# Performance work log

Hardware: AMD Instinct MI355X
Metric: run time of the kernel (lower is better)

## Reference

```python
import jax, jax.numpy as jnp
import numpy as np

EMB, HID, E, TOPK = 1024, 4096, 8, 2

def setup_inputs() -> dict:
    key = jax.random.key(0)
    ks = jax.random.split(key, 10)
    s = 0.02
    return {
        "x":   jax.random.normal(ks[0], (4, 2048, EMB), jnp.float32),
        # router MLP: Linear(EMB,HID) -> SiLU -> Linear(HID,E)
        "rw1": s * jax.random.normal(ks[1], (EMB, HID), jnp.float32),
        "rb1": jnp.zeros((HID,), jnp.float32),
        "rw2": s * jax.random.normal(ks[2], (HID, E), jnp.float32),
        "rb2": jnp.zeros((E,), jnp.float32),
        # stacked expert MLPs: Linear(EMB,HID) -> SiLU -> Linear(HID,EMB)
        "w1":  s * jax.random.normal(ks[3], (E, EMB, HID), jnp.float32),
        "b1":  jnp.zeros((E, HID), jnp.float32),
        "w2":  s * jax.random.normal(ks[4], (E, HID, EMB), jnp.float32),
        "b2":  jnp.zeros((E, EMB), jnp.float32),
    }

def reference(x, rw1, rb1, rw2, rb2, w1, b1, w2, b2):
    B, S, D = x.shape
    # Router: logits over experts, top-k, softmax over the k selected logits
    logits = jax.nn.silu(jnp.einsum('bsd,dh->bsh', x, rw1) + rb1)
    logits = jnp.einsum('bsh,he->bse', logits, rw2) + rb2
    k_logits, k_index = jax.lax.top_k(logits, TOPK)          # [B,S,K]
    k_prob = jax.nn.softmax(k_logits, axis=-1)               # [B,S,K]

    xf = x.reshape(B * S, D)                                 # [T,D]
    k_index_f = k_index.reshape(B * S, TOPK)
    k_prob_f = k_prob.reshape(B * S, TOPK)

    out = jnp.zeros_like(xf)
    for e in range(E):  # small fixed expert count
        # per-token combine weight for expert e (0 if not routed)
        we = jnp.sum(jnp.where(k_index_f == e, k_prob_f, 0.0), axis=-1)  # [T]
        h = jax.nn.silu(xf @ w1[e] + b1[e]) @ w2[e] + b2[e]              # [T,D]
        out = out + we[:, None] * h
    return out.reshape(B, S, D)
```

## Files before the change

kernel.cpp:

```cpp
#include <hip/hip_runtime.h>
#include <stdint.h>

#define TOK 8192
#define EMBD 1024
#define HIDD 4096
#define NEXP 8

typedef _Float16 f16;
typedef _Float16 f16x8 __attribute__((ext_vector_type(8)));
typedef _Float16 f16x4 __attribute__((ext_vector_type(4)));
typedef float f32x4 __attribute__((ext_vector_type(4)));
typedef unsigned short u16;
typedef unsigned short u16x4 __attribute__((ext_vector_type(4)));

constexpr size_t OFF_X16   = 0;
constexpr size_t OFF_RW1T  = OFF_X16  + (size_t)TOK*EMBD*2;
constexpr size_t OFF_W1T   = OFF_RW1T + (size_t)HIDD*EMBD*2;
constexpr size_t OFF_W2T   = OFF_W1T  + (size_t)NEXP*HIDD*EMBD*2;
constexpr size_t OFF_HR    = OFF_W2T  + (size_t)NEXP*EMBD*HIDD*2;
constexpr size_t OFF_HG    = OFF_HR   + (size_t)TOK*HIDD*2;
constexpr size_t OFF_YG    = OFF_HG   + (size_t)(2*TOK+256)*HIDD*2;
constexpr size_t OFF_XF    = OFF_YG   + (size_t)(2*TOK+256)*EMBD*2;
constexpr size_t OFF_HF    = OFF_XF   + 512UL*EMBD*4;
constexpr size_t OFF_KIDX  = OFF_HF   + 512UL*HIDD*4;
constexpr size_t OFF_KW    = OFF_KIDX + 2UL*TOK*4;
constexpr size_t OFF_RMAP  = OFF_KW   + 2UL*TOK*4;
constexpr size_t OFF_TMAP  = OFF_RMAP + 2UL*TOK*4;
constexpr size_t OFF_FLAG  = OFF_TMAP + 2UL*TOK*4;
constexpr size_t OFF_MISC  = OFF_FLAG + 512UL*4;
constexpr size_t OFF_RW2T  = OFF_MISC + 1024;
constexpr size_t WS_TOTAL  = OFF_RW2T + (size_t)NEXP*HIDD*2;

__device__ __align__(1024) unsigned char g_ws[WS_TOTAL];

__device__ __forceinline__ u16 f2h(float f) {
  f16 h = (f16)f;
  return __builtin_bit_cast(u16, h);
}

__device__ __forceinline__ void async_cp16(const void* g, void* l) {
  __builtin_amdgcn_global_load_lds((const __attribute__((address_space(1))) void*)g,
                                   (__attribute__((address_space(3))) void*)l, 16, 0, 0);
}

__global__ void k_prep(const float* __restrict__ x, const float* __restrict__ rw2) {
  int b = blockIdx.x, tid = threadIdx.x;
  constexpr int NBX = TOK * EMBD / 1024;
  if (b < NBX) {
    u16* X16 = (u16*)(g_ws + OFF_X16);
    int i = (b * 256 + tid) * 4;
    float4 v = *(const float4*)(x + i);
    u16x4 o;
    o[0] = f2h(v.x); o[1] = f2h(v.y); o[2] = f2h(v.z); o[3] = f2h(v.w);
    *(u16x4*)(X16 + i) = o;
  } else if (b < NBX + HIDD / 256) {
    u16* RW2T = (u16*)(g_ws + OFF_RW2T);
    int h = (b - NBX) * 256 + tid;
    float4 a = *(const float4*)&rw2[(size_t)h * 8];
    float4 bb = *(const float4*)&rw2[(size_t)h * 8 + 4];
    RW2T[0 * HIDD + h] = f2h(a.x);
    RW2T[1 * HIDD + h] = f2h(a.y);
    RW2T[2 * HIDD + h] = f2h(a.z);
    RW2T[3 * HIDD + h] = f2h(a.w);
    RW2T[4 * HIDD + h] = f2h(bb.x);
    RW2T[5 * HIDD + h] = f2h(bb.y);
    RW2T[6 * HIDD + h] = f2h(bb.z);
    RW2T[7 * HIDD + h] = f2h(bb.w);
  } else {
    if (tid < 32) ((int*)(g_ws + OFF_MISC))[tid] = 0;
  }
}

template <int R, int C>
__device__ __forceinline__ void tpose(const float* __restrict__ src, u16* __restrict__ dst,
                                      int bx, int by, u16 (*t)[68]) {
  int r0 = by * 64, c0 = bx * 64;
  int tid = threadIdx.x;
#pragma unroll
  for (int i = 0; i < 4; ++i) {
    int r = i * 16 + (tid >> 4);
    int c4 = (tid & 15) * 4;
    float4 v = *(const float4*)&src[(size_t)(r0 + r) * C + c0 + c4];
    u16x4 p;
    p[0] = f2h(v.x); p[1] = f2h(v.y); p[2] = f2h(v.z); p[3] = f2h(v.w);
    *(u16x4*)&t[r][c4 ^ (((r >> 2) & 15) << 2)] = p;
  }
  __syncthreads();
#pragma unroll
  for (int i = 0; i < 4; ++i) {
    int lin = i * 256 + tid;
    int cc = lin >> 4;
    int q = lin & 15;
    int rr0 = q * 4;
    int cs = cc ^ (q << 2);
    u16x4 o;
    o[0] = t[rr0 + 0][cs];
    o[1] = t[rr0 + 1][cs];
    o[2] = t[rr0 + 2][cs];
    o[3] = t[rr0 + 3][cs];
    *(u16x4*)&dst[(size_t)(c0 + cc) * R + r0 + rr0] = o;
  }
}

__global__ void k_transpose_all(const float* __restrict__ rw1, const float* __restrict__ w1,
                                const float* __restrict__ w2) {
  __shared__ u16 t[64][68];
  int flat = blockIdx.x;
  if (flat < 9 * 1024) {
    int m = flat >> 10, rem = flat & 1023;
    int bx = rem & 63, by = rem >> 6;
    const float* src = (m == 0) ? rw1 : w1 + (size_t)(m - 1) * EMBD * HIDD;
    u16* dst = (u16*)(g_ws + OFF_RW1T) + (size_t)m * HIDD * EMBD;
    tpose<EMBD, HIDD>(src, dst, bx, by, t);
  } else {
    int f2 = flat - 9 * 1024;
    int m = f2 >> 10, rem = f2 & 1023;
    int bx = rem & 15, by = rem >> 4;
    const float* src = w2 + (size_t)m * HIDD * EMBD;
    u16* dst = (u16*)(g_ws + OFF_W2T) + (size_t)m * EMBD * HIDD;
    tpose<HIDD, EMBD>(src, dst, bx, by, t);
  }
}

template <bool SILU, bool GROUPED, bool INDIRECT, int GN>
__global__ __launch_bounds__(512, 2) void gemm256(size_t offA, size_t offB,
                                                  const float* __restrict__ bias,
                                                  size_t offC, int Mfix, int N, int K) {
  const u16* A  = (const u16*)(g_ws + offA);
  const u16* BT = (const u16*)(g_ws + offB);
  u16* C = (u16*)(g_ws + offC);
  const int* offs = (const int*)(g_ws + OFF_MISC) + 8;
  const int* tokmap = (const int*)(g_ws + OFF_TMAP);

  int nx = gridDim.x, ny = gridDim.y;
  int nwg = nx * ny * gridDim.z;
  int flat = (blockIdx.z * ny + blockIdx.y) * nx + blockIdx.x;
  int cpx = nwg >> 3;
  int u = (flat & 7) * cpx + (flat >> 3);
  int bxin = u % GN;
  int t1 = u / GN;
  int by = t1 % ny;
  int t2 = t1 / ny;
  int nxg = nx / GN;
  int g = t2 % nxg;
  int bz = t2 / nxg;
  int bx = g * GN + bxin;

  int e = GROUPED ? bz : 0;
  int rbase = GROUPED ? offs[e] : 0;
  int Me = GROUPED ? (offs[e + 1] - rbase) : Mfix;
  int m0 = by * 256;
  if (m0 >= Me) return;
  int n0 = bx * 256;
  const u16* Be = BT + (size_t)e * N * K;
  const float* be = bias + (size_t)e * N;

  __shared__ __align__(128) u16 SM[65536];

  int tid = threadIdx.x;
  int lane = tid & 63, wid = tid >> 6;
  int wm = wid >> 2, wn = wid & 3;
  int rsel = lane & 15;
  int rg = lane >> 4;
  int sp0 = (rg ^ (rsel & 7)) * 8;

  int srow = tid >> 3;
  int cnom = tid & 7;
  int csrc = (cnom ^ (srow & 7)) * 8;

  const u16* aP[4];
  const u16* bP[4];
#pragma unroll
  for (int i = 0; i < 4; ++i) {
    int r = m0 + i * 64 + srow;
    if (GROUPED) r = (r < Me) ? r : (Me - 1);
    if (INDIRECT) aP[i] = A + (size_t)tokmap[rbase + r] * K + csrc;
    else          aP[i] = A + (size_t)(rbase + r) * K + csrc;
    bP[i] = Be + (size_t)(n0 + i * 64 + srow) * K + csrc;
  }

#define STAGE(b, k0)                                                        \
  do {                                                                      \
    _Pragma("unroll") for (int i = 0; i < 4; ++i)                           \
      async_cp16(aP[i] + (k0), &SM[(b)*16384 + (i * 512 + tid) * 8]);       \
    _Pragma("unroll") for (int i = 0; i < 4; ++i)                           \
      async_cp16(bP[i] + (k0), &SM[32768 + (b)*16384 + (i * 512 + tid) * 8]); \
  } while (0)

#define COMPUTE(bb)                                                             \
  {                                                                             \
    const u16* Ab = &SM[(bb)*16384];                                            \
    const u16* Bb = &SM[32768 + (bb)*16384];                                    \
    _Pragma("unroll") for (int ks = 0; ks < 2; ++ks) {                          \
      int spo = sp0 ^ (ks << 5);                                                \
      f16x8 af[8], bf[4];                                                       \
      _Pragma("unroll") for (int i = 0; i < 8; ++i)                             \
        af[i] = *(const f16x8*)&Ab[wm * 8192 + i * 1024 + rsel * 64 + spo];     \
      _Pragma("unroll") for (int j = 0; j < 4; ++j)                             \
        bf[j] = *(const f16x8*)&Bb[wn * 4096 + j * 1024 + rsel * 64 + spo];     \
      _Pragma("unroll") for (int i = 0; i < 8; ++i)                             \
        _Pragma("unroll") for (int j = 0; j < 4; ++j)                           \
          acc[i][j] = __builtin_amdgcn_mfma_f32_16x16x32_f16(af[i], bf[j],      \
                                                             acc[i][j], 0, 0, 0); \
    }                                                                           \
  }

  f32x4 acc[8][4] = {};
  int nt = K >> 6;

  STAGE(0, 0);
  asm volatile("s_waitcnt vmcnt(0)" ::: "memory");
  __builtin_amdgcn_s_barrier();

  int buf = 0;
  for (int t = 0; t < nt; ++t) {
    if (t + 1 < nt) STAGE(buf ^ 1, (t + 1) << 6);
    COMPUTE(buf);
    asm volatile("s_waitcnt vmcnt(0)" ::: "memory");
    __builtin_amdgcn_s_barrier();
    buf ^= 1;
  }
#undef COMPUTE
#undef STAGE

  u16* Cs = SM;
#pragma unroll
  for (int j = 0; j < 4; ++j) {
    int colL = wn * 64 + j * 16 + rsel;
    float bn = be[n0 + colL];
#pragma unroll
    for (int i = 0; i < 8; ++i) {
#pragma unroll
      for (int r = 0; r < 4; ++r) {
        int ml = wm * 128 + i * 16 + rg * 4 + r;
        float v = acc[i][j][r] + bn;
        if (SILU) v = v / (1.0f + __expf(-v));
        Cs[ml * 256 + colL] = f2h(v);
      }
    }
  }
  __syncthreads();
#pragma unroll
  for (int i = 0; i < 16; ++i) {
    int lin = i * 512 + tid;
    int row = lin >> 5, sl = lin & 31;
    if (!GROUPED || (m0 + row < Me))
      *(uint4*)(C + (size_t)(rbase + m0 + row) * N + n0 + sl * 8) =
          *(const uint4*)&Cs[row * 256 + sl * 8];
  }
}

__global__ void k_router(const float* __restrict__ rb2, const float* __restrict__ x) {
  const u16* HR = (const u16*)(g_ws + OFF_HR);
  const u16* RW2T = (const u16*)(g_ws + OFF_RW2T);
  int* kidx = (int*)(g_ws + OFF_KIDX);
  float* kw = (float*)(g_ws + OFF_KW);
  int* flag = (int*)(g_ws + OFF_FLAG);
  float* XF = (float*)(g_ws + OFF_XF);
  int* misc = (int*)(g_ws + OFF_MISC);

  int t = blockIdx.x, tid = threadIdx.x;
  int lane = tid & 63, w = tid >> 6;
  float acc[8] = {};
  const u16* hrow = HR + (size_t)t * HIDD;
#pragma unroll
  for (int i = 0; i < 2; ++i) {
    int base = i * 2048 + tid * 8;
    f16x8 v = *(const f16x8*)&hrow[base];
    float hv[8];
#pragma unroll
    for (int jj = 0; jj < 8; ++jj) hv[jj] = (float)v[jj];
#pragma unroll
    for (int e2 = 0; e2 < 8; ++e2) {
      f16x8 wv = *(const f16x8*)&RW2T[e2 * HIDD + base];
#pragma unroll
      for (int jj = 0; jj < 8; ++jj) acc[e2] += hv[jj] * (float)wv[jj];
    }
  }
#pragma unroll
  for (int m = 1; m < 64; m <<= 1)
#pragma unroll
    for (int e2 = 0; e2 < 8; ++e2) acc[e2] += __shfl_xor(acc[e2], m);

  __shared__ float red[4][8];
  __shared__ int s_fi;
  if (lane == 0)
    for (int e2 = 0; e2 < 8; ++e2) red[w][e2] = acc[e2];
  if (tid == 0) s_fi = -1;
  __syncthreads();
  if (tid == 0) {
    float lg[8];
    for (int e2 = 0; e2 < 8; ++e2)
      lg[e2] = red[0][e2] + red[1][e2] + red[2][e2] + red[3][e2] + rb2[e2];
    int i1 = 0; float l1 = lg[0];
    for (int e2 = 1; e2 < 8; ++e2) if (lg[e2] > l1) { l1 = lg[e2]; i1 = e2; }
    int i2 = -1; float l2 = -3.4e38f;
    for (int e2 = 0; e2 < 8; ++e2) if (e2 != i1 && lg[e2] > l2) { l2 = lg[e2]; i2 = e2; }
    float l3 = -3.4e38f;
    for (int e2 = 0; e2 < 8; ++e2) if (e2 != i1 && e2 != i2 && lg[e2] > l3) l3 = lg[e2];
    float ex = __expf(l2 - l1);
    float inv = 1.0f / (1.0f + ex);
    kidx[2 * t] = i1; kidx[2 * t + 1] = i2;
    kw[2 * t] = inv;  kw[2 * t + 1] = ex * inv;
    if (l2 - l3 < 4e-3f) {
      int fi = atomicAdd(misc + 30, 1);
      if (fi < 512) { flag[fi] = t; s_fi = fi; }
    }
  }
  __syncthreads();
  int fi = s_fi;
  if (fi >= 0) {
    const float* xs = x + (size_t)t * EMBD;
    float* xd = XF + (size_t)fi * EMBD;
    int d = tid * 4;
    *(float4*)(xd + d) = *(const float4*)(xs + d);
  }
}

__global__ __launch_bounds__(256) void k_flag_gemm(const float* __restrict__ rw1,
                                                   const float* __restrict__ rb1) {
  int* misc = (int*)(g_ws + OFF_MISC);
  int F = misc[30]; if (F > 512) F = 512;
  int m0 = blockIdx.y * 64;
  if (m0 >= F) return;
  int n0 = blockIdx.x * 64;
  const float* XF = (const float*)(g_ws + OFF_XF);
  float* HF = (float*)(g_ws + OFF_HF);
  __shared__ float As[64][17];
  __shared__ float Bs[16][65];
  int tid = threadIdx.x;
  float acc[4][4] = {};
  for (int k0 = 0; k0 < EMBD; k0 += 16) {
#pragma unroll
    for (int i = 0; i < 4; ++i) {
      int lin = i * 256 + tid;
      As[lin >> 4][lin & 15] = XF[(size_t)(m0 + (lin >> 4)) * EMBD + k0 + (lin & 15)];
      Bs[lin >> 6][lin & 63] = rw1[(size_t)(k0 + (lin >> 6)) * HIDD + n0 + (lin & 63)];
    }
    __syncthreads();
    int ty = tid >> 4, tx = tid & 15;
#pragma unroll
    for (int kk = 0; kk < 16; ++kk) {
      float a4[4], b4[4];
#pragma unroll
      for (int a = 0; a < 4; ++a) a4[a] = As[ty * 4 + a][kk];
#pragma unroll
      for (int b = 0; b < 4; ++b) b4[b] = Bs[kk][tx * 4 + b];
#pragma unroll
      for (int a = 0; a < 4; ++a)
#pragma unroll
        for (int b = 0; b < 4; ++b) acc[a][b] += a4[a] * b4[b];
    }
    __syncthreads();
  }
  int ty = tid >> 4, tx = tid & 15;
  for (int a = 0; a < 4; ++a)
    for (int b = 0; b < 4; ++b) {
      int n = n0 + tx * 4 + b;
      float v = acc[a][b] + rb1[n];
      v = v / (1.0f + __expf(-v));
      HF[(size_t)(m0 + ty * 4 + a) * HIDD + n] = v;
    }
}

__global__ void k_flag_fix(const float* __restrict__ rw2, const float* __restrict__ rb2) {
  int* misc = (int*)(g_ws + OFF_MISC);
  int F = misc[30]; if (F > 512) F = 512;
  int fi = blockIdx.x; if (fi >= F) return;
  const int* flag = (const int*)(g_ws + OFF_FLAG);
  const float* HF = (const float*)(g_ws + OFF_HF);
  int* kidx = (int*)(g_ws + OFF_KIDX);
  float* kw = (float*)(g_ws + OFF_KW);
  int t = flag[fi];
  int tid = threadIdx.x, lane = tid & 63, w = tid >> 6;
  const float* h = HF + (size_t)fi * HIDD;
  float acc[8] = {};
  for (int i = 0; i < 16; ++i) {
    int hh = i * 256 + tid;
    float hv = h[hh];
    const float* r2 = rw2 + (size_t)hh * 8;
#pragma unroll
    for (int e2 = 0; e2 < 8; ++e2) acc[e2] += hv * r2[e2];
  }
#pragma unroll
  for (int m = 1; m < 64; m <<= 1)
#pragma unroll
    for (int e2 = 0; e2 < 8; ++e2) acc[e2] += __shfl_xor(acc[e2], m);
  __shared__ float red[4][8];
  if (lane == 0)
    for (int e2 = 0; e2 < 8; ++e2) red[w][e2] = acc[e2];
  __syncthreads();
  if (tid == 0) {
    float lg[8];
    for (int e2 = 0; e2 < 8; ++e2)
      lg[e2] = red[0][e2] + red[1][e2] + red[2][e2] + red[3][e2] + rb2[e2];
    int i1 = 0; float l1 = lg[0];
    for (int e2 = 1; e2 < 8; ++e2) if (lg[e2] > l1) { l1 = lg[e2]; i1 = e2; }
    int i2 = -1; float l2 = -3.4e38f;
    for (int e2 = 0; e2 < 8; ++e2) if (e2 != i1 && lg[e2] > l2) { l2 = lg[e2]; i2 = e2; }
    float ex = __expf(l2 - l1);
    float inv = 1.0f / (1.0f + ex);
    kidx[2 * t] = i1; kidx[2 * t + 1] = i2;
    kw[2 * t] = inv;  kw[2 * t + 1] = ex * inv;
  }
}

__global__ __launch_bounds__(1024) void k_count_scan() {
  const int* kidx = (const int*)(g_ws + OFF_KIDX);
  int* misc = (int*)(g_ws + OFF_MISC);
  int tid = threadIdx.x;
  int c[8] = {};
  for (int i = tid; i < 2 * TOK; i += 1024) {
    int e = kidx[i];
#pragma unroll
    for (int k = 0; k < 8; ++k) c[k] += (e == k) ? 1 : 0;
  }
#pragma unroll
  for (int m = 1; m < 64; m <<= 1)
#pragma unroll
    for (int k = 0; k < 8; ++k) c[k] += __shfl_xor(c[k], m);
  __shared__ int red[16][8];
  int lane = tid & 63, w = tid >> 6;
  if (lane == 0)
#pragma unroll
    for (int k = 0; k < 8; ++k) red[w][k] = c[k];
  __syncthreads();
  if (tid == 0) {
    int* offs = misc + 8;
    int* cur = misc + 20;
    offs[0] = 0;
    for (int e = 0; e < 8; ++e) {
      int s = 0;
      for (int ww = 0; ww < 16; ++ww) s += red[ww][e];
      offs[e + 1] = offs[e] + s;
      cur[e] = offs[e];
    }
  }
}

__global__ void k_build() {
  int s = blockIdx.x * 256 + threadIdx.x;
  if (s < 2 * TOK) {
    const int* kidx = (const int*)(g_ws + OFF_KIDX);
    int* rowmap = (int*)(g_ws + OFF_RMAP);
    int* tokmap = (int*)(g_ws + OFF_TMAP);
    int* misc = (int*)(g_ws + OFF_MISC);
    int e = kidx[s];
    int r = atomicAdd(&misc[20 + e], 1);
    rowmap[s] = r;
    tokmap[r] = s >> 1;
  }
}

__global__ void k_combine(float* __restrict__ out) {
  int t = blockIdx.x, tid = threadIdx.x;
  const int* rowmap = (const int*)(g_ws + OFF_RMAP);
  const float* kw = (const float*)(g_ws + OFF_KW);
  const u16* YG = (const u16*)(g_ws + OFF_YG);
  int r0 = rowmap[2 * t], r1 = rowmap[2 * t + 1];
  float w0 = kw[2 * t], w1 = kw[2 * t + 1];
  int d = tid * 4;
  f16x4 a = *(const f16x4*)(YG + (size_t)r0 * EMBD + d);
  f16x4 b = *(const f16x4*)(YG + (size_t)r1 * EMBD + d);
  float4 o;
  o.x = w0 * (float)a[0] + w1 * (float)b[0];
  o.y = w0 * (float)a[1] + w1 * (float)b[1];
  o.z = w0 * (float)a[2] + w1 * (float)b[2];
  o.w = w0 * (float)a[3] + w1 * (float)b[3];
  *(float4*)(out + (size_t)t * EMBD + d) = o;
}

extern "C" void kernel_launch(void* const* d_in, const int* in_sizes, int n_in,
                              void* d_out, int out_size, void* d_ws, size_t ws_size,
                              hipStream_t stream) {
  const float* x   = (const float*)d_in[0];
  const float* rw1 = (const float*)d_in[1];
  const float* rb1 = (const float*)d_in[2];
  const float* rw2 = (const float*)d_in[3];
  const float* rb2 = (const float*)d_in[4];
  const float* w1  = (const float*)d_in[5];
  const float* b1  = (const float*)d_in[6];
  const float* w2  = (const float*)d_in[7];
  const float* b2  = (const float*)d_in[8];
  float* out = (float*)d_out;

  k_prep<<<dim3(TOK * EMBD / 1024 + HIDD / 256 + 1), dim3(256), 0, stream>>>(x, rw2);
  k_transpose_all<<<dim3(9 * 1024 + 8 * 1024), dim3(256), 0, stream>>>(rw1, w1, w2);
  gemm256<true, false, false, 4><<<dim3(HIDD / 256, TOK / 256, 1), dim3(512), 0, stream>>>(
      OFF_X16, OFF_RW1T, rb1, OFF_HR, TOK, HIDD, EMBD);
  k_router<<<dim3(TOK), dim3(256), 0, stream>>>(rb2, x);
  k_flag_gemm<<<dim3(HIDD / 64, 8), dim3(256), 0, stream>>>(rw1, rb1);
  k_flag_fix<<<dim3(512), dim3(256), 0, stream>>>(rw2, rb2);
  k_count_scan<<<dim3(1), dim3(1024), 0, stream>>>();
  k_build<<<dim3(2 * TOK / 256), dim3(256), 0, stream>>>();
  gemm256<true, true, true, 4><<<dim3(HIDD / 256, 2 * TOK / 256, 8), dim3(512), 0, stream>>>(
      OFF_X16, OFF_W1T, b1, OFF_HG, 0, HIDD, EMBD);
  gemm256<false, true, false, 1><<<dim3(EMBD / 256, 2 * TOK / 256, 8), dim3(512), 0, stream>>>(
      OFF_HG, OFF_W2T, b2, OFF_YG, 0, EMBD, HIDD);
  k_combine<<<dim3(TOK), dim3(256), 0, stream>>>(out);
}
```

Measured before the change: 810.7 us.

## Fuse router second linear into first router GEMM epilogue with partial logits

The router's HID->E projection now runs in the epilogue of the first router GEMM on the f16 tile already in LDS. Each block writes per-column-block partial logits instead of writing the full hidden activation to global memory. k_router becomes a light per-token kernel that sums 16 partials and does top-2. The flagged-token GEMM also reads x through the flag index instead of a copied buffer. This removes a large global write and reread of the router hidden activations, at the cost of a serial dot-product epilogue in the GEMM.

```diff
diff --git a/kernel.cpp b/kernel.cpp
--- a/kernel.cpp
+++ b/kernel.cpp
@@ -29,7 +29,8 @@
 constexpr size_t OFF_FLAG  = OFF_TMAP + 2UL*TOK*4;
 constexpr size_t OFF_MISC  = OFF_FLAG + 512UL*4;
 constexpr size_t OFF_RW2T  = OFF_MISC + 1024;
-constexpr size_t WS_TOTAL  = OFF_RW2T + (size_t)NEXP*HIDD*2;
+constexpr size_t OFF_LG    = OFF_RW2T + (size_t)NEXP*HIDD*2;
+constexpr size_t WS_TOTAL  = OFF_LG + 16UL*TOK*8*4;
 
 __device__ __align__(1024) unsigned char g_ws[WS_TOTAL];
 
@@ -122,7 +123,7 @@
   }
 }
 
-template <bool SILU, bool GROUPED, bool INDIRECT, int GN>
+template <bool SILU, bool GROUPED, bool INDIRECT, int GN, bool ROUTER>
 __global__ __launch_bounds__(512, 2) void gemm256(size_t offA, size_t offB,
                                                   const float* __restrict__ bias,
                                                   size_t offC, int Mfix, int N, int K) {
@@ -240,91 +241,97 @@
     }
   }
   __syncthreads();
-#pragma unroll
-  for (int i = 0; i < 16; ++i) {
-    int lin = i * 512 + tid;
-    int row = lin >> 5, sl = lin & 31;
-    if (!GROUPED || (m0 + row < Me))
-      *(uint4*)(C + (size_t)(rbase + m0 + row) * N + n0 + sl * 8) =
-          *(const uint4*)&Cs[row * 256 + sl * 8];
-  }
-}
-
-__global__ void k_router(const float* __restrict__ rb2, const float* __restrict__ x) {
-  const u16* HR = (const u16*)(g_ws + OFF_HR);
-  const u16* RW2T = (const u16*)(g_ws + OFF_RW2T);
+
+  if constexpr (ROUTER) {
+    float* LG = (float*)(g_ws + OFF_LG);
+    const u16* RW2T = (const u16*)(g_ws + OFF_RW2T);
+    int row = tid >> 1, half = tid & 1;
+    int cbase = half * 128;
+    int rot = (lane >> 1) & 15;
+    float a8[8];
+#pragma unroll
+    for (int ee = 0; ee < 8; ++ee) a8[ee] = 0.f;
+#pragma unroll
+    for (int ee = 0; ee < 8; ++ee) {
+      const u16* wrow = &RW2T[ee * HIDD + n0 + cbase];
+      float a = 0.f;
+      for (int i = 0; i < 16; ++i) {
+        int c8 = (i + rot) & 15;
+        f16x8 wv = *(const f16x8*)&wrow[c8 * 8];
+        f16x8 cv = *(const f16x8*)&Cs[row * 256 + cbase + c8 * 8];
+#pragma unroll
+        for (int j = 0; j < 8; ++j) a += (float)cv[j] * (float)wv[j];
+      }
+      a8[ee] = a;
+    }
+#pragma unroll
+    for (int ee = 0; ee < 8; ++ee) a8[ee] += __shfl_xor(a8[ee], 1);
+    if (half == 0) {
+      float* dst = LG + ((size_t)bx * TOK + (m0 + row)) * 8;
+      f32x4 lo, hi;
+      lo[0] = a8[0]; lo[1] = a8[1]; lo[2] = a8[2]; lo[3] = a8[3];
+      hi[0] = a8[4]; hi[1] = a8[5]; hi[2] = a8[6]; hi[3] = a8[7];
+      *(f32x4*)dst = lo;
+      *(f32x4*)(dst + 4) = hi;
+    }
+  } else {
+#pragma unroll
+    for (int i = 0; i < 16; ++i) {
+      int lin = i * 512 + tid;
+      int row = lin >> 5, sl = lin & 31;
+      if (!GROUPED || (m0 + row < Me))
+        *(uint4*)(C + (size_t)(rbase + m0 + row) * N + n0 + sl * 8) =
+            *(const uint4*)&Cs[row * 256 + sl * 8];
+    }
+  }
+}
+
+__global__ void k_router(const float* __restrict__ rb2) {
+  const float* LG = (const float*)(g_ws + OFF_LG);
   int* kidx = (int*)(g_ws + OFF_KIDX);
   float* kw = (float*)(g_ws + OFF_KW);
   int* flag = (int*)(g_ws + OFF_FLAG);
-  float* XF = (float*)(g_ws + OFF_XF);
   int* misc = (int*)(g_ws + OFF_MISC);
 
-  int t = blockIdx.x, tid = threadIdx.x;
-  int lane = tid & 63, w = tid >> 6;
-  float acc[8] = {};
-  const u16* hrow = HR + (size_t)t * HIDD;
-#pragma unroll
-  for (int i = 0; i < 2; ++i) {
-    int base = i * 2048 + tid * 8;
-    f16x8 v = *(const f16x8*)&hrow[base];
-    float hv[8];
-#pragma unroll
-    for (int jj = 0; jj < 8; ++jj) hv[jj] = (float)v[jj];
-#pragma unroll
-    for (int e2 = 0; e2 < 8; ++e2) {
-      f16x8 wv = *(const f16x8*)&RW2T[e2 * HIDD + base];
-#pragma unroll
-      for (int jj = 0; jj < 8; ++jj) acc[e2] += hv[jj] * (float)wv[jj];
-    }
-  }
-#pragma unroll
-  for (int m = 1; m < 64; m <<= 1)
-#pragma unroll
-    for (int e2 = 0; e2 < 8; ++e2) acc[e2] += __shfl_xor(acc[e2], m);
-
-  __shared__ float red[4][8];
-  __shared__ int s_fi;
-  if (lane == 0)
-    for (int e2 = 0; e2 < 8; ++e2) red[w][e2] = acc[e2];
-  if (tid == 0) s_fi = -1;
-  __syncthreads();
-  if (tid == 0) {
-    float lg[8];
-    for (int e2 = 0; e2 < 8; ++e2)
-      lg[e2] = red[0][e2] + red[1][e2] + red[2][e2] + red[3][e2] + rb2[e2];
-    int i1 = 0; float l1 = lg[0];
-    for (int e2 = 1; e2 < 8; ++e2) if (lg[e2] > l1) { l1 = lg[e2]; i1 = e2; }
-    int i2 = -1; float l2 = -3.4e38f;
-    for (int e2 = 0; e2 < 8; ++e2) if (e2 != i1 && lg[e2] > l2) { l2 = lg[e2]; i2 = e2; }
-    float l3 = -3.4e38f;
-    for (int e2 = 0; e2 < 8; ++e2) if (e2 != i1 && e2 != i2 && lg[e2] > l3) l3 = lg[e2];
-    float ex = __expf(l2 - l1);
-    float inv = 1.0f / (1.0f + ex);
-    kidx[2 * t] = i1; kidx[2 * t + 1] = i2;
-    kw[2 * t] = inv;  kw[2 * t + 1] = ex * inv;
-    if (l2 - l3 < 4e-3f) {
-      int fi = atomicAdd(misc + 30, 1);
-      if (fi < 512) { flag[fi] = t; s_fi = fi; }
-    }
-  }
-  __syncthreads();
-  int fi = s_fi;
-  if (fi >= 0) {
-    const float* xs = x + (size_t)t * EMBD;
-    float* xd = XF + (size_t)fi * EMBD;
-    int d = tid * 4;
-    *(float4*)(xd + d) = *(const float4*)(xs + d);
+  int t = blockIdx.x * 256 + threadIdx.x;
+  float lg[8];
+#pragma unroll
+  for (int e2 = 0; e2 < 8; ++e2) lg[e2] = rb2[e2];
+  for (int p = 0; p < 16; ++p) {
+    const float* src = LG + ((size_t)p * TOK + t) * 8;
+    f32x4 a = *(const f32x4*)src;
+    f32x4 b = *(const f32x4*)(src + 4);
+    lg[0] += a[0]; lg[1] += a[1]; lg[2] += a[2]; lg[3] += a[3];
+    lg[4] += b[0]; lg[5] += b[1]; lg[6] += b[2]; lg[7] += b[3];
+  }
+  int i1 = 0; float l1 = lg[0];
+#pragma unroll
+  for (int e2 = 1; e2 < 8; ++e2) if (lg[e2] > l1) { l1 = lg[e2]; i1 = e2; }
+  int i2 = -1; float l2 = -3.4e38f;
+#pragma unroll
+  for (int e2 = 0; e2 < 8; ++e2) if (e2 != i1 && lg[e2] > l2) { l2 = lg[e2]; i2 = e2; }
+  float l3 = -3.4e38f;
+#pragma unroll
+  for (int e2 = 0; e2 < 8; ++e2) if (e2 != i1 && e2 != i2 && lg[e2] > l3) l3 = lg[e2];
+  float ex = __expf(l2 - l1);
+  float inv = 1.0f / (1.0f + ex);
+  kidx[2 * t] = i1; kidx[2 * t + 1] = i2;
+  kw[2 * t] = inv;  kw[2 * t + 1] = ex * inv;
+  if (l2 - l3 < 4e-3f) {
+    int fi = atomicAdd(misc + 30, 1);
+    if (fi < 512) flag[fi] = t;
   }
 }
 
 __global__ __launch_bounds__(256) void k_flag_gemm(const float* __restrict__ rw1,
-                                                   const float* __restrict__ rb1) {
+                                                   const float* __restrict__ rb1,
+                                                   const float* __restrict__ x) {
   int* misc = (int*)(g_ws + OFF_MISC);
+  const int* flag = (const int*)(g_ws + OFF_FLAG);
   int F = misc[30]; if (F > 512) F = 512;
   int m0 = blockIdx.y * 64;
   if (m0 >= F) return;
   int n0 = blockIdx.x * 64;
-  const float* XF = (const float*)(g_ws + OFF_XF);
   float* HF = (float*)(g_ws + OFF_HF);
   __shared__ float As[64][17];
   __shared__ float Bs[16][65];
@@ -334,7 +341,9 @@
 #pragma unroll
     for (int i = 0; i < 4; ++i) {
       int lin = i * 256 + tid;
-      As[lin >> 4][lin & 15] = XF[(size_t)(m0 + (lin >> 4)) * EMBD + k0 + (lin & 15)];
+      int rowf = m0 + (lin >> 4);
+      int tok = flag[rowf < F ? rowf : 0];
+      As[lin >> 4][lin & 15] = x[(size_t)tok * EMBD + k0 + (lin & 15)];
       Bs[lin >> 6][lin & 63] = rw1[(size_t)(k0 + (lin >> 6)) * HIDD + n0 + (lin & 63)];
     }
     __syncthreads();
@@ -486,16 +495,16 @@
 
   k_prep<<<dim3(TOK * EMBD / 1024 + HIDD / 256 + 1), dim3(256), 0, stream>>>(x, rw2);
   k_transpose_all<<<dim3(9 * 1024 + 8 * 1024), dim3(256), 0, stream>>>(rw1, w1, w2);
-  gemm256<true, false, false, 4><<<dim3(HIDD / 256, TOK / 256, 1), dim3(512), 0, stream>>>(
+  gemm256<true, false, false, 4, true><<<dim3(HIDD / 256, TOK / 256, 1), dim3(512), 0, stream>>>(
       OFF_X16, OFF_RW1T, rb1, OFF_HR, TOK, HIDD, EMBD);
-  k_router<<<dim3(TOK), dim3(256), 0, stream>>>(rb2, x);
-  k_flag_gemm<<<dim3(HIDD / 64, 8), dim3(256), 0, stream>>>(rw1, rb1);
+  k_router<<<dim3(TOK / 256), dim3(256), 0, stream>>>(rb2);
+  k_flag_gemm<<<dim3(HIDD / 64, 8), dim3(256), 0, stream>>>(rw1, rb1, x);
   k_flag_fix<<<dim3(512), dim3(256), 0, stream>>>(rw2, rb2);
   k_count_scan<<<dim3(1), dim3(1024), 0, stream>>>();
   k_build<<<dim3(2 * TOK / 256), dim3(256), 0, stream>>>();
-  gemm256<true, true, true, 4><<<dim3(HIDD / 256, 2 * TOK / 256, 8), dim3(512), 0, stream>>>(
+  gemm256<true, true, true, 4, false><<<dim3(HIDD / 256, 2 * TOK / 256, 8), dim3(512), 0, stream>>>(
       OFF_X16, OFF_W1T, b1, OFF_HG, 0, HIDD, EMBD);
-  gemm256<false, true, false, 1><<<dim3(EMBD / 256, 2 * TOK / 256, 8), dim3(512), 0, stream>>>(
+  gemm256<false, true, false, 1, false><<<dim3(EMBD / 256, 2 * TOK / 256, 8), dim3(512), 0, stream>>>(
       OFF_HG, OFF_W2T, b2, OFF_YG, 0, EMBD, HIDD);
   k_combine<<<dim3(TOK), dim3(256), 0, stream>>>(out);
 }
```

Result: slower. 932.8 us (+15.1%).
